# Optimization experiments

Hardware: AMD Instinct MI355X
Metric: run time of the kernel (lower is better)

## Reference

```python
import jax, jax.numpy as jnp
import numpy as np

LAG = 1  # from init_kwargs

def _from_embedding(z, lag):
    # torch loop: out[i] = z[i] for i < lag; out[i] = z[i] + detach(out[i-lag]) otherwise.
    # For i grouped by residue class mod lag this is a cumulative sum along dim 0.
    # The detach means gradients flow only through the direct z[i] term (identity grad),
    # so forward = cumsum, and we restore detach semantics with stop_gradient.
    N = z.shape[0]
    assert N % lag == 0, "sequence length must be a multiple of lag"
    zg = z.reshape(N // lag, lag, *z.shape[1:])        # [G, lag, B, D]
    cum = jnp.cumsum(zg, axis=0).reshape(z.shape)       # [N, B, D]
    # forward value = cum; backward: d(out)/d(z) = identity (accumulated prefix detached)
    return jax.lax.stop_gradient(cum - z) + z

def setup_inputs() -> dict:
    key = jax.random.key(0)
    k1, = jax.random.split(key, 1)
    z = jax.random.normal(k1, (8192, 64, 128), dtype=jnp.float32)
    previous_loss = jnp.zeros((1,), dtype=jnp.float32)
    return {"z": z, "previous_loss": previous_loss}

def reference(z, previous_loss):
    z_delagged = _from_embedding(z, LAG)
    return (z_delagged, previous_loss)
```

## Files before the change

kernel.cpp:

```cpp
#include <hip/hip_runtime.h>


typedef float f4 __attribute__((ext_vector_type(4)));

constexpr int NROWS = 8192;
constexpr int NCOLS = 8192;
constexpr int NCOL4 = NCOLS / 4;
constexpr int TPB   = 256;
constexpr int KCH   = 128;
constexpr int RR    = NROWS / KCH;
constexpr int CT    = NCOL4 / TPB;

__global__ __launch_bounds__(TPB) void k_partial(const f4* __restrict__ z,
                                                 f4* __restrict__ part) {
    const int tile  = blockIdx.x & (CT - 1);
    const int chunk = blockIdx.x >> 3;
    const int c4    = tile * TPB + threadIdx.x;
    const f4* p = z + (size_t)chunk * RR * NCOL4 + c4;
    f4 a = (f4)0.f;
    #pragma unroll 8
    for (int r = 0; r < RR; ++r) a += p[(size_t)r * NCOL4];
    part[(size_t)chunk * NCOL4 + c4] = a;
}

__global__ __launch_bounds__(TPB) void k_scan(float* __restrict__ part,
                                              const float* __restrict__ prev,
                                              float* __restrict__ out_tail) {
    const int c = blockIdx.x * TPB + threadIdx.x;
    float run = 0.f;
    #pragma unroll 16
    for (int k = 0; k < KCH; ++k) {
        const size_t i = (size_t)k * NCOLS + c;
        float v = part[i];
        part[i] = run;
        run += v;
    }
    if (blockIdx.x == 0 && threadIdx.x == 0) out_tail[0] = prev[0];
}

__global__ __launch_bounds__(TPB) void k_apply(const f4* __restrict__ z,
                                               const f4* __restrict__ part,
                                               f4* __restrict__ out) {
    const int tile  = blockIdx.x & (CT - 1);
    const int chunk = KCH - 1 - (blockIdx.x >> 3);
    const int c4    = tile * TPB + threadIdx.x;
    f4 a = part[(size_t)chunk * NCOL4 + c4];
    const f4* p = z   + (size_t)chunk * RR * NCOL4 + c4;
    f4*       q = out + (size_t)chunk * RR * NCOL4 + c4;
    #pragma unroll 4
    for (int r = 0; r < RR; ++r) {
        a += p[(size_t)r * NCOL4];
        __builtin_nontemporal_store(a, &q[(size_t)r * NCOL4]);
    }
}

extern "C" void kernel_launch(void* const* d_in, const int* in_sizes, int n_in,
                              void* d_out, int out_size, void* d_ws, size_t ws_size,
                              hipStream_t stream) {
    const f4*    z    = (const f4*)d_in[0];
    const float* prev = (const float*)d_in[1];
    float*       out  = (float*)d_out;
    float*       part = (float*)d_ws;
    float*       tail = out + (size_t)NROWS * NCOLS;

    k_partial<<<KCH * CT, TPB, 0, stream>>>(z, (f4*)part);
    k_scan<<<NCOLS / TPB, TPB, 0, stream>>>(part, prev, tail);
    k_apply<<<KCH * CT, TPB, 0, stream>>>(z, (const f4*)part, (f4*)out);
}
```

Before: 136.6 us.

## Drop scan kernel; compute chunk prefix redundantly in apply kernel

Removes the middle k_scan launch that serially scanned the per-chunk partial sums. Each k_apply block now sums all preceding chunk aggregates for its columns directly, so its exclusive prefix is computed redundantly. This saves a kernel launch and a serial dependency step. In exchange the total aggregate reads grow quadratically with the chunk count (about 32 MB spread over blocks, largely L2-resident), and later chunks get extra latency.

New measurement: 139.0 us. Within noise of the previous version (+1.8%).

```diff
diff --git a/kernel.cpp b/kernel.cpp
--- a/kernel.cpp
+++ b/kernel.cpp
@@ -12,45 +12,38 @@
 constexpr int CT    = NCOL4 / TPB;
 
 __global__ __launch_bounds__(TPB) void k_partial(const f4* __restrict__ z,
-                                                 f4* __restrict__ part) {
+                                                 f4* __restrict__ agg,
+                                                 const float* __restrict__ prev,
+                                                 float* __restrict__ out_tail) {
     const int tile  = blockIdx.x & (CT - 1);
     const int chunk = blockIdx.x >> 3;
     const int c4    = tile * TPB + threadIdx.x;
+    if (blockIdx.x == 0 && threadIdx.x == 0) out_tail[0] = prev[0];
     const f4* p = z + (size_t)chunk * RR * NCOL4 + c4;
     f4 a = (f4)0.f;
     #pragma unroll 8
     for (int r = 0; r < RR; ++r) a += p[(size_t)r * NCOL4];
-    part[(size_t)chunk * NCOL4 + c4] = a;
-}
-
-__global__ __launch_bounds__(TPB) void k_scan(float* __restrict__ part,
-                                              const float* __restrict__ prev,
-                                              float* __restrict__ out_tail) {
-    const int c = blockIdx.x * TPB + threadIdx.x;
-    float run = 0.f;
-    #pragma unroll 16
-    for (int k = 0; k < KCH; ++k) {
-        const size_t i = (size_t)k * NCOLS + c;
-        float v = part[i];
-        part[i] = run;
-        run += v;
-    }
-    if (blockIdx.x == 0 && threadIdx.x == 0) out_tail[0] = prev[0];
+    agg[(size_t)chunk * NCOL4 + c4] = a;
 }
 
 __global__ __launch_bounds__(TPB) void k_apply(const f4* __restrict__ z,
-                                               const f4* __restrict__ part,
+                                               const f4* __restrict__ agg,
                                                f4* __restrict__ out) {
     const int tile  = blockIdx.x & (CT - 1);
     const int chunk = KCH - 1 - (blockIdx.x >> 3);
     const int c4    = tile * TPB + threadIdx.x;
-    f4 a = part[(size_t)chunk * NCOL4 + c4];
+
+    f4 s = (f4)0.f;
+    const f4* ap = agg + c4;
+    #pragma unroll 8
+    for (int cp = 0; cp < chunk; ++cp) s += ap[(size_t)cp * NCOL4];
+
     const f4* p = z   + (size_t)chunk * RR * NCOL4 + c4;
     f4*       q = out + (size_t)chunk * RR * NCOL4 + c4;
     #pragma unroll 4
     for (int r = 0; r < RR; ++r) {
-        a += p[(size_t)r * NCOL4];
-        __builtin_nontemporal_store(a, &q[(size_t)r * NCOL4]);
+        s += p[(size_t)r * NCOL4];
+        __builtin_nontemporal_store(s, &q[(size_t)r * NCOL4]);
     }
 }
 
@@ -60,10 +53,9 @@
     const f4*    z    = (const f4*)d_in[0];
     const float* prev = (const float*)d_in[1];
     float*       out  = (float*)d_out;
-    float*       part = (float*)d_ws;
     float*       tail = out + (size_t)NROWS * NCOLS;
+    f4*          agg  = (f4*)d_ws;
 
-    k_partial<<<KCH * CT, TPB, 0, stream>>>(z, (f4*)part);
-    k_scan<<<NCOLS / TPB, TPB, 0, stream>>>(part, prev, tail);
-    k_apply<<<KCH * CT, TPB, 0, stream>>>(z, (const f4*)part, (f4*)out);
+    k_partial<<<KCH * CT, TPB, 0, stream>>>(z, agg, prev, tail);
+    k_apply<<<KCH * CT, TPB, 0, stream>>>(z, (const f4*)agg, (f4*)out);
 }
```
